# Optimization experiments

Measured on AMD Instinct MI355X. Metric: run time of the kernel, lower is better.

## Reference

```python
import jax, jax.numpy as jnp
import numpy as np

N_NODES = 100000
N_GRAPHS = 512
NEG_SLOPE = 0.2


def gat_layer(x, src, dst, W, a_src, a_dst, b):
    # PyG GATConv (heads=1, concat=True, add_self_loops handled by caller via src/dst)
    h = x @ W                                   # [N, F]
    e = jax.nn.leaky_relu((h @ a_src)[src] + (h @ a_dst)[dst], NEG_SLOPE)  # [E]
    m = jax.ops.segment_max(e, dst, num_segments=N_NODES)
    ex = jnp.exp(e - m[dst])
    s = jax.ops.segment_sum(ex, dst, num_segments=N_NODES)
    alpha = ex / (s[dst] + 1e-16)               # per-destination softmax
    out = jax.ops.segment_sum(alpha[:, None] * h[src], dst, num_segments=N_NODES)
    return out + b


def setup_inputs() -> dict:
    key = jax.random.key(0)
    ks = jax.random.split(key, 12)
    x = jax.random.normal(ks[0], (N_NODES, 5), dtype=jnp.float32)
    edge_index = jax.random.randint(ks[1], (2, 3200000), 0, N_NODES, dtype=jnp.int64)
    batch = jnp.sort(jax.random.randint(ks[2], (N_NODES,), 0, N_GRAPHS, dtype=jnp.int64))
    def glorot(k, shape):
        lim = float(np.sqrt(6.0 / (shape[0] + shape[-1])))
        return jax.random.uniform(k, shape, jnp.float32, -lim, lim)
    return {
        "x": x, "edge_index": edge_index, "batch": batch,
        "W1": glorot(ks[3], (5, 16)), "as1": glorot(ks[4], (16,)), "ad1": glorot(ks[5], (16,)), "b1": jnp.zeros((16,), jnp.float32),
        "W2": glorot(ks[6], (16, 16)), "as2": glorot(ks[7], (16,)), "ad2": glorot(ks[8], (16,)), "b2": jnp.zeros((16,), jnp.float32),
        "Wf": glorot(ks[9], (16, 2)), "bf": jnp.zeros((2,), jnp.float32),
    }


def reference(x, edge_index, batch, W1, as1, ad1, b1, W2, as2, ad2, b2, Wf, bf):
    # add self-loops (PyG GATConv default)
    loop = jnp.arange(N_NODES, dtype=edge_index.dtype)
    src = jnp.concatenate([edge_index[0], loop])
    dst = jnp.concatenate([edge_index[1], loop])
    h = jax.nn.relu(gat_layer(x, src, dst, W1, as1, ad1, b1))
    h = jax.nn.relu(gat_layer(h, src, dst, W2, as2, ad2, b2))
    # global mean pool over graphs
    sums = jax.ops.segment_sum(h, batch, num_segments=N_GRAPHS)
    cnt = jax.ops.segment_sum(jnp.ones((N_NODES,), h.dtype), batch, num_segments=N_GRAPHS)
    pooled = sums / jnp.maximum(cnt, 1.0)[:, None]   # [G, 16]
    return pooled @ Wf + bf                          # [G, 2]
```

## Files before the change

### kernel.cpp

```cpp
#include <hip/hip_runtime.h>
#include <math.h>

#define N_NODES 100000
#define N_GRAPHS 512
#define F 16
#define NEG_SLOPE 0.2f
#define DMAX 80
#define NSLOT 64
#define NBUCK 391
#define BCAP 8704
#define EPB 16

__device__ __forceinline__ float lrelu(float v) {
    return v > 0.0f ? v : NEG_SLOPE * v;
}

__device__ __forceinline__ unsigned fkey(float f) {
    unsigned b = __float_as_uint(f);
    return (b & 0x80000000u) ? ~b : (b | 0x80000000u);
}
__device__ __forceinline__ float funkey(unsigned k) {
    unsigned b = (k & 0x80000000u) ? (k ^ 0x80000000u) : ~k;
    return __uint_as_float(b);
}

__global__ void k_prep1(const float* __restrict__ x,
                        const float* __restrict__ W1,
                        const float* __restrict__ as1,
                        const float* __restrict__ ad1,
                        float* __restrict__ h1,
                        float* __restrict__ ssrc,
                        float* __restrict__ sdst,
                        unsigned* __restrict__ cs1,
                        unsigned* __restrict__ cd1) {
    int n = blockIdx.x * blockDim.x + threadIdx.x;
    float ss = -INFINITY, sd = -INFINITY;
    if (n < N_NODES) {
        float xi[5];
#pragma unroll
        for (int i = 0; i < 5; ++i) xi[i] = x[n * 5 + i];
        ss = 0.f; sd = 0.f;
#pragma unroll
        for (int f = 0; f < F; ++f) {
            float acc = 0.f;
#pragma unroll
            for (int i = 0; i < 5; ++i) acc += xi[i] * W1[i * F + f];
            h1[n * F + f] = acc;
            ss += acc * as1[f];
            sd += acc * ad1[f];
        }
        ssrc[n] = ss;
        sdst[n] = sd;
    }
    unsigned ks = fkey(ss), kd = fkey(sd);
#pragma unroll
    for (int off = 32; off; off >>= 1) {
        ks = max(ks, (unsigned)__shfl_xor((int)ks, off, 64));
        kd = max(kd, (unsigned)__shfl_xor((int)kd, off, 64));
    }
    __shared__ unsigned ls[4], ld[4];
    int wid = threadIdx.x >> 6, lane = threadIdx.x & 63;
    if (lane == 0) { ls[wid] = ks; ld[wid] = kd; }
    __syncthreads();
    if (threadIdx.x == 0) {
        unsigned ms = ls[0], md = ld[0];
#pragma unroll
        for (int w = 1; w < 4; ++w) { ms = max(ms, ls[w]); md = max(md, ld[w]); }
        atomicMax(&cs1[blockIdx.x & (NSLOT - 1)], ms);
        atomicMax(&cd1[blockIdx.x & (NSLOT - 1)], md);
    }
}

__global__ void k_part(const int* __restrict__ esrc,
                       const int* __restrict__ edst, int E0,
                       int* __restrict__ bcur,
                       unsigned* __restrict__ bucket) {
    __shared__ int hist[NBUCK];
    __shared__ int gbase[NBUCK];
    __shared__ int off[NBUCK];
    int tbase = blockIdx.x * (blockDim.x * EPB);

    for (int i = threadIdx.x; i < NBUCK; i += blockDim.x) hist[i] = 0;
    __syncthreads();

    int rb[EPB];
    unsigned rv[EPB];
#pragma unroll
    for (int i = 0; i < EPB; ++i) {
        int e = tbase + i * blockDim.x + threadIdx.x;
        rb[i] = -1;
        if (e < E0) {
            int d = edst[e];
            int s = esrc[e];
            int b = d >> 8;
            rb[i] = b;
            rv[i] = (unsigned)s | ((unsigned)(d & 255) << 17);
            atomicAdd(&hist[b], 1);
        }
    }
    __syncthreads();

    for (int b = threadIdx.x; b < NBUCK; b += blockDim.x) {
        int h = hist[b];
        gbase[b] = h ? atomicAdd(&bcur[b], h) : 0;
        off[b] = 0;
    }
    __syncthreads();

#pragma unroll
    for (int i = 0; i < EPB; ++i) {
        int b = rb[i];
        if (b >= 0) {
            int p = gbase[b] + atomicAdd(&off[b], 1);
            if (p < BCAP) bucket[(size_t)b * BCAP + p] = rv[i];
        }
    }
}

__global__ void k_fill2(const int* __restrict__ bcur,
                        const unsigned* __restrict__ bucket,
                        int* __restrict__ col,
                        int* __restrict__ deg) {
    int b = blockIdx.x;
    __shared__ int cur[256];
    if (threadIdx.x < 256) cur[threadIdx.x] = 0;
    __syncthreads();
    int cnt = min(bcur[b], BCAP);
    const unsigned* bk = bucket + (size_t)b * BCAP;
    for (int i = threadIdx.x; i < cnt; i += blockDim.x) {
        unsigned v = __builtin_nontemporal_load(&bk[i]);
        int s = (int)(v & 0x1FFFFu);
        int dl = (int)(v >> 17);
        int r = atomicAdd(&cur[dl], 1);
        if (r < DMAX) col[((size_t)((b << 8) | dl)) * DMAX + r] = s;
    }
    __syncthreads();
    if (threadIdx.x < 256) {
        int dst = (b << 8) | threadIdx.x;
        if (dst < N_NODES) deg[dst] = min(cur[threadIdx.x], DMAX);
    }
}

__device__ __forceinline__ float gat_aggregate(int n, int lane,
                                               const int* __restrict__ deg,
                                               const int* __restrict__ col,
                                               const float* __restrict__ ssrc,
                                               const float* __restrict__ sdst,
                                               const float* __restrict__ h,
                                               const float* __restrict__ b,
                                               float c) {
    int dg = deg[n];
    size_t st = (size_t)n * DMAX;
    float sd = sdst[n];
    float acc = 0.f, ssum = 0.f;
    for (int base = 0; base < dg; base += 16) {
        int j = base + lane;
        float pe = 0.f;
        int src = 0;
        if (j < dg) {
            src = __builtin_nontemporal_load(&col[st + j]);
            pe = __expf(lrelu(ssrc[src] + sd) - c);
        }
        ssum += pe;
        int cnt = min(16, dg - base);
        for (int k = 0; k < cnt; ++k) {
            int sk = __shfl(src, k, 16);
            float pk = __shfl(pe, k, 16);
            acc += pk * h[sk * F + lane];
        }
    }
#pragma unroll
    for (int off = 8; off; off >>= 1) ssum += __shfl_xor(ssum, off, 16);
    float pes = __expf(lrelu(ssrc[n] + sd) - c);
    ssum += pes;
    acc += pes * h[n * F + lane];
    float of = acc / (ssum + 1e-16f) + b[lane];
    return of > 0.f ? of : 0.f;
}

__device__ __forceinline__ float slot_max_c(const unsigned* __restrict__ cs,
                                            const unsigned* __restrict__ cd) {
    unsigned ms = 0, md = 0;
#pragma unroll 8
    for (int i = 0; i < NSLOT; ++i) {
        ms = max(ms, cs[i]);
        md = max(md, cd[i]);
    }
    return lrelu(funkey(ms) + funkey(md));
}

__global__ void k_gather1(const int* __restrict__ deg,
                          const int* __restrict__ col,
                          const float* __restrict__ ssrc1,
                          const float* __restrict__ sdst1,
                          const float* __restrict__ h1,
                          const float* __restrict__ b1,
                          const float* __restrict__ W2,
                          const float* __restrict__ as2,
                          const float* __restrict__ ad2,
                          float* __restrict__ h2,
                          float* __restrict__ ssrc2,
                          float* __restrict__ sdst2,
                          const unsigned* __restrict__ cs1,
                          const unsigned* __restrict__ cd1,
                          unsigned* __restrict__ cs2,
                          unsigned* __restrict__ cd2) {
    int n = blockIdx.x * (blockDim.x >> 4) + (threadIdx.x >> 4);
    int lane = threadIdx.x & 15;
    float c1 = slot_max_c(cs1, cd1);
    float ho = gat_aggregate(n, lane, deg, col, ssrc1, sdst1, h1, b1, c1);

    float h2f = 0.f;
#pragma unroll
    for (int i = 0; i < F; ++i) {
        float hoi = __shfl(ho, i, 16);
        h2f += hoi * W2[i * F + lane];
    }
    h2[n * F + lane] = h2f;

    float ps = h2f * as2[lane];
    float pd = h2f * ad2[lane];
#pragma unroll
    for (int off = 8; off; off >>= 1) {
        ps += __shfl_xor(ps, off, 16);
        pd += __shfl_xor(pd, off, 16);
    }
    if (lane == 0) { ssrc2[n] = ps; sdst2[n] = pd; }

    unsigned ks = fkey(ps), kd = fkey(pd);
#pragma unroll
    for (int off = 32; off; off >>= 1) {
        ks = max(ks, (unsigned)__shfl_xor((int)ks, off, 64));
        kd = max(kd, (unsigned)__shfl_xor((int)kd, off, 64));
    }
    __shared__ unsigned ls[4], ld[4];
    int wid = threadIdx.x >> 6, wl = threadIdx.x & 63;
    if (wl == 0) { ls[wid] = ks; ld[wid] = kd; }
    __syncthreads();
    if (threadIdx.x == 0) {
        unsigned ms = ls[0], md = ld[0];
#pragma unroll
        for (int w = 1; w < 4; ++w) { ms = max(ms, ls[w]); md = max(md, ld[w]); }
        atomicMax(&cs2[blockIdx.x & (NSLOT - 1)], ms);
        atomicMax(&cd2[blockIdx.x & (NSLOT - 1)], md);
    }
}

__global__ void k_gather2(const int* __restrict__ deg,
                          const int* __restrict__ col,
                          const float* __restrict__ ssrc2,
                          const float* __restrict__ sdst2,
                          const float* __restrict__ h2,
                          const float* __restrict__ b2,
                          const int* __restrict__ batch,
                          float* __restrict__ gsum,
                          float* __restrict__ gcnt,
                          const unsigned* __restrict__ cs2,
                          const unsigned* __restrict__ cd2) {
    __shared__ float pool[4 * F];
    __shared__ float pcnt[4];
    if (threadIdx.x < 4 * F) pool[threadIdx.x] = 0.f;
    if (threadIdx.x < 4) pcnt[threadIdx.x] = 0.f;
    __syncthreads();

    int n = blockIdx.x * (blockDim.x >> 4) + (threadIdx.x >> 4);
    int lane = threadIdx.x & 15;
    float c2 = slot_max_c(cs2, cd2);
    float ho = gat_aggregate(n, lane, deg, col, ssrc2, sdst2, h2, b2, c2);

    int g = batch[n];
    int g0 = batch[blockIdx.x * (blockDim.x >> 4)];
    int idx = g - g0;
    if (idx < 4) {
        atomicAdd(&pool[idx * F + lane], ho);
        if (lane == 0) atomicAdd(&pcnt[idx], 1.f);
    } else {
        atomicAdd(&gsum[g * F + lane], ho);
        if (lane == 0) atomicAdd(&gcnt[g], 1.f);
    }
    __syncthreads();
    if (threadIdx.x < 4 * F) {
        float v = pool[threadIdx.x];
        if (v != 0.f)
            atomicAdd(&gsum[(g0 + (threadIdx.x >> 4)) * F + (threadIdx.x & 15)], v);
    }
    if (threadIdx.x < 4) {
        float cv = pcnt[threadIdx.x];
        if (cv != 0.f) atomicAdd(&gcnt[g0 + threadIdx.x], cv);
    }
}

__global__ void k_final(const float* __restrict__ gsum,
                        const float* __restrict__ gcnt,
                        const float* __restrict__ Wf,
                        const float* __restrict__ bf,
                        float* __restrict__ out) {
    int g = blockIdx.x * blockDim.x + threadIdx.x;
    if (g >= N_GRAPHS) return;
    float inv = 1.f / fmaxf(gcnt[g], 1.f);
    float o0 = bf[0], o1 = bf[1];
#pragma unroll
    for (int i = 0; i < F; ++i) {
        float p = gsum[g * F + i] * inv;
        o0 += p * Wf[i * 2 + 0];
        o1 += p * Wf[i * 2 + 1];
    }
    out[g * 2 + 0] = o0;
    out[g * 2 + 1] = o1;
}

extern "C" void kernel_launch(void* const* d_in, const int* in_sizes, int n_in,
                              void* d_out, int out_size, void* d_ws, size_t ws_size,
                              hipStream_t stream) {
    const float* x   = (const float*)d_in[0];
    const int*   ei  = (const int*)d_in[1];
    const int*   bat = (const int*)d_in[2];
    const float* W1  = (const float*)d_in[3];
    const float* as1 = (const float*)d_in[4];
    const float* ad1 = (const float*)d_in[5];
    const float* b1  = (const float*)d_in[6];
    const float* W2  = (const float*)d_in[7];
    const float* as2 = (const float*)d_in[8];
    const float* ad2 = (const float*)d_in[9];
    const float* b2  = (const float*)d_in[10];
    const float* Wf  = (const float*)d_in[11];
    const float* bf  = (const float*)d_in[12];
    float* out = (float*)d_out;

    const int E0 = in_sizes[1] / 2;
    const int* esrc = ei;
    const int* edst = ei + E0;

    float* fws   = (float*)d_ws;
    float* h1    = fws;
    float* h2    = h1 + (size_t)N_NODES * F;
    float* ssrc1 = h2 + (size_t)N_NODES * F;
    float* sdst1 = ssrc1 + N_NODES;
    float* ssrc2 = sdst1 + N_NODES;
    float* sdst2 = ssrc2 + N_NODES;
    int*   col   = (int*)(sdst2 + N_NODES);
    int*   deg   = col + (size_t)N_NODES * DMAX;
    unsigned* bucket = (unsigned*)(deg + N_NODES);
    int*      zbase = (int*)(bucket + (size_t)NBUCK * BCAP);
    int*      bcur  = zbase;
    unsigned* cs1   = (unsigned*)(bcur + NBUCK);
    unsigned* cd1   = cs1 + NSLOT;
    unsigned* cs2   = cd1 + NSLOT;
    unsigned* cd2   = cs2 + NSLOT;
    float*    gsum  = (float*)(cd2 + NSLOT);
    float*    gcnt  = gsum + (size_t)N_GRAPHS * F;
    size_t zbytes = (size_t)(NBUCK + 4 * NSLOT + N_GRAPHS * F + N_GRAPHS) * 4;

    hipMemsetAsync(zbase, 0, zbytes, stream);

    const int BT = 256;
    dim3 bN((N_NODES + BT - 1) / BT);
    dim3 bT((E0 + BT * EPB - 1) / (BT * EPB));
    dim3 bB(NBUCK);
    dim3 bG16((N_NODES * 16) / BT);
    dim3 bG((N_GRAPHS + BT - 1) / BT);

    k_prep1<<<bN, BT, 0, stream>>>(x, W1, as1, ad1, h1, ssrc1, sdst1, cs1, cd1);
    k_part<<<bT, BT, 0, stream>>>(esrc, edst, E0, bcur, bucket);
    k_fill2<<<bB, 1024, 0, stream>>>(bcur, bucket, col, deg);
    k_gather1<<<bG16, BT, 0, stream>>>(deg, col, ssrc1, sdst1, h1, b1,
                                       W2, as2, ad2, h2, ssrc2, sdst2,
                                       cs1, cd1, cs2, cd2);
    k_gather2<<<bG16, BT, 0, stream>>>(deg, col, ssrc2, sdst2, h2, b2,
                                       bat, gsum, gcnt, cs2, cd2);
    k_final<<<bG, BT, 0, stream>>>(gsum, gcnt, Wf, bf, out);
}
```

Before: 330.2 us.

## Use wave-per-node float4 gather aggregation and fuse prep into partition kernel

```diff
diff --git a/kernel.cpp b/kernel.cpp
--- a/kernel.cpp
+++ b/kernel.cpp
@@ -24,95 +24,96 @@
     return __uint_as_float(b);
 }
 
-__global__ void k_prep1(const float* __restrict__ x,
-                        const float* __restrict__ W1,
-                        const float* __restrict__ as1,
-                        const float* __restrict__ ad1,
-                        float* __restrict__ h1,
-                        float* __restrict__ ssrc,
-                        float* __restrict__ sdst,
-                        unsigned* __restrict__ cs1,
-                        unsigned* __restrict__ cd1) {
-    int n = blockIdx.x * blockDim.x + threadIdx.x;
-    float ss = -INFINITY, sd = -INFINITY;
-    if (n < N_NODES) {
-        float xi[5];
-#pragma unroll
-        for (int i = 0; i < 5; ++i) xi[i] = x[n * 5 + i];
-        ss = 0.f; sd = 0.f;
-#pragma unroll
-        for (int f = 0; f < F; ++f) {
-            float acc = 0.f;
-#pragma unroll
-            for (int i = 0; i < 5; ++i) acc += xi[i] * W1[i * F + f];
-            h1[n * F + f] = acc;
-            ss += acc * as1[f];
-            sd += acc * ad1[f];
-        }
-        ssrc[n] = ss;
-        sdst[n] = sd;
-    }
-    unsigned ks = fkey(ss), kd = fkey(sd);
-#pragma unroll
-    for (int off = 32; off; off >>= 1) {
-        ks = max(ks, (unsigned)__shfl_xor((int)ks, off, 64));
-        kd = max(kd, (unsigned)__shfl_xor((int)kd, off, 64));
-    }
-    __shared__ unsigned ls[4], ld[4];
-    int wid = threadIdx.x >> 6, lane = threadIdx.x & 63;
-    if (lane == 0) { ls[wid] = ks; ld[wid] = kd; }
-    __syncthreads();
-    if (threadIdx.x == 0) {
-        unsigned ms = ls[0], md = ld[0];
-#pragma unroll
-        for (int w = 1; w < 4; ++w) { ms = max(ms, ls[w]); md = max(md, ld[w]); }
-        atomicMax(&cs1[blockIdx.x & (NSLOT - 1)], ms);
-        atomicMax(&cd1[blockIdx.x & (NSLOT - 1)], md);
-    }
-}
-
-__global__ void k_part(const int* __restrict__ esrc,
-                       const int* __restrict__ edst, int E0,
-                       int* __restrict__ bcur,
-                       unsigned* __restrict__ bucket) {
+__global__ void k_part_prep(const int* __restrict__ esrc,
+                            const int* __restrict__ edst, int E0, int nT,
+                            int* __restrict__ bcur,
+                            unsigned* __restrict__ bucket,
+                            const float* __restrict__ x,
+                            const float* __restrict__ W1,
+                            const float* __restrict__ as1,
+                            const float* __restrict__ ad1,
+                            float* __restrict__ h1,
+                            float* __restrict__ ssrc,
+                            float* __restrict__ sdst,
+                            unsigned* __restrict__ cs1,
+                            unsigned* __restrict__ cd1) {
     __shared__ int hist[NBUCK];
     __shared__ int gbase[NBUCK];
     __shared__ int off[NBUCK];
-    int tbase = blockIdx.x * (blockDim.x * EPB);
-
-    for (int i = threadIdx.x; i < NBUCK; i += blockDim.x) hist[i] = 0;
-    __syncthreads();
-
-    int rb[EPB];
-    unsigned rv[EPB];
-#pragma unroll
-    for (int i = 0; i < EPB; ++i) {
-        int e = tbase + i * blockDim.x + threadIdx.x;
-        rb[i] = -1;
-        if (e < E0) {
-            int d = edst[e];
-            int s = esrc[e];
-            int b = d >> 8;
-            rb[i] = b;
-            rv[i] = (unsigned)s | ((unsigned)(d & 255) << 17);
-            atomicAdd(&hist[b], 1);
-        }
-    }
-    __syncthreads();
-
-    for (int b = threadIdx.x; b < NBUCK; b += blockDim.x) {
-        int h = hist[b];
-        gbase[b] = h ? atomicAdd(&bcur[b], h) : 0;
-        off[b] = 0;
-    }
-    __syncthreads();
-
-#pragma unroll
-    for (int i = 0; i < EPB; ++i) {
-        int b = rb[i];
-        if (b >= 0) {
-            int p = gbase[b] + atomicAdd(&off[b], 1);
-            if (p < BCAP) bucket[(size_t)b * BCAP + p] = rv[i];
+    __shared__ unsigned ls[4], ld[4];
+
+    if ((int)blockIdx.x < nT) {
+        int tbase = blockIdx.x * (blockDim.x * EPB);
+        for (int i = threadIdx.x; i < NBUCK; i += blockDim.x) hist[i] = 0;
+        __syncthreads();
+
+        int rb[EPB];
+        unsigned rv[EPB];
+#pragma unroll
+        for (int i = 0; i < EPB; ++i) {
+            int e = tbase + i * blockDim.x + threadIdx.x;
+            rb[i] = -1;
+            if (e < E0) {
+                int d = edst[e];
+                int s = esrc[e];
+                int b = d >> 8;
+                rb[i] = b;
+                rv[i] = (unsigned)s | ((unsigned)(d & 255) << 17);
+                atomicAdd(&hist[b], 1);
+            }
+        }
+        __syncthreads();
+
+        for (int b = threadIdx.x; b < NBUCK; b += blockDim.x) {
+            int h = hist[b];
+            gbase[b] = h ? atomicAdd(&bcur[b], h) : 0;
+            off[b] = 0;
+        }
+        __syncthreads();
+
+#pragma unroll
+        for (int i = 0; i < EPB; ++i) {
+            int b = rb[i];
+            if (b >= 0) {
+                int p = gbase[b] + atomicAdd(&off[b], 1);
+                if (p < BCAP) bucket[(size_t)b * BCAP + p] = rv[i];
+            }
+        }
+    } else {
+        int n = (blockIdx.x - nT) * blockDim.x + threadIdx.x;
+        float ss = -INFINITY, sd = -INFINITY;
+        if (n < N_NODES) {
+            float xi[5];
+#pragma unroll
+            for (int i = 0; i < 5; ++i) xi[i] = x[n * 5 + i];
+            ss = 0.f; sd = 0.f;
+#pragma unroll
+            for (int f = 0; f < F; ++f) {
+                float acc = 0.f;
+#pragma unroll
+                for (int i = 0; i < 5; ++i) acc += xi[i] * W1[i * F + f];
+                h1[n * F + f] = acc;
+                ss += acc * as1[f];
+                sd += acc * ad1[f];
+            }
+            ssrc[n] = ss;
+            sdst[n] = sd;
+        }
+        unsigned ks = fkey(ss), kd = fkey(sd);
+#pragma unroll
+        for (int o = 32; o; o >>= 1) {
+            ks = max(ks, (unsigned)__shfl_xor((int)ks, o, 64));
+            kd = max(kd, (unsigned)__shfl_xor((int)kd, o, 64));
+        }
+        int wid = threadIdx.x >> 6, lane = threadIdx.x & 63;
+        if (lane == 0) { ls[wid] = ks; ld[wid] = kd; }
+        __syncthreads();
+        if (threadIdx.x == 0) {
+            unsigned ms = ls[0], md = ld[0];
+#pragma unroll
+            for (int w = 1; w < 4; ++w) { ms = max(ms, ls[w]); md = max(md, ld[w]); }
+            atomicMax(&cs1[blockIdx.x & (NSLOT - 1)], ms);
+            atomicMax(&cd1[blockIdx.x & (NSLOT - 1)], md);
         }
     }
 }
@@ -141,41 +142,55 @@
     }
 }
 
-__device__ __forceinline__ float gat_aggregate(int n, int lane,
+__device__ __forceinline__ float4 gat_agg_wave(int n, int eslot, int quad,
                                                const int* __restrict__ deg,
                                                const int* __restrict__ col,
                                                const float* __restrict__ ssrc,
                                                const float* __restrict__ sdst,
-                                               const float* __restrict__ h,
+                                               const float4* __restrict__ h4,
                                                const float* __restrict__ b,
                                                float c) {
     int dg = deg[n];
     size_t st = (size_t)n * DMAX;
     float sd = sdst[n];
-    float acc = 0.f, ssum = 0.f;
+    float4 acc = make_float4(0.f, 0.f, 0.f, 0.f);
+    float psum = 0.f;
     for (int base = 0; base < dg; base += 16) {
-        int j = base + lane;
-        float pe = 0.f;
-        int src = 0;
+        int j = base + eslot;
         if (j < dg) {
-            src = __builtin_nontemporal_load(&col[st + j]);
-            pe = __expf(lrelu(ssrc[src] + sd) - c);
-        }
-        ssum += pe;
-        int cnt = min(16, dg - base);
-        for (int k = 0; k < cnt; ++k) {
-            int sk = __shfl(src, k, 16);
-            float pk = __shfl(pe, k, 16);
-            acc += pk * h[sk * F + lane];
-        }
-    }
-#pragma unroll
-    for (int off = 8; off; off >>= 1) ssum += __shfl_xor(ssum, off, 16);
+            int src = __builtin_nontemporal_load(&col[st + j]);
+            float pe = __expf(lrelu(ssrc[src] + sd) - c);
+            float4 hv = h4[(size_t)src * 4 + quad];
+            acc.x += pe * hv.x;
+            acc.y += pe * hv.y;
+            acc.z += pe * hv.z;
+            acc.w += pe * hv.w;
+            psum += pe;
+        }
+    }
+#pragma unroll
+    for (int o = 4; o < 64; o <<= 1) {
+        acc.x += __shfl_xor(acc.x, o, 64);
+        acc.y += __shfl_xor(acc.y, o, 64);
+        acc.z += __shfl_xor(acc.z, o, 64);
+        acc.w += __shfl_xor(acc.w, o, 64);
+        psum  += __shfl_xor(psum, o, 64);
+    }
     float pes = __expf(lrelu(ssrc[n] + sd) - c);
-    ssum += pes;
-    acc += pes * h[n * F + lane];
-    float of = acc / (ssum + 1e-16f) + b[lane];
-    return of > 0.f ? of : 0.f;
+    float4 hv = h4[(size_t)n * 4 + quad];
+    acc.x += pes * hv.x;
+    acc.y += pes * hv.y;
+    acc.z += pes * hv.z;
+    acc.w += pes * hv.w;
+    psum += pes;
+    float inv = 1.f / (psum + 1e-16f);
+    const float4 bq = ((const float4*)b)[quad];
+    float4 of;
+    of.x = fmaxf(acc.x * inv + bq.x, 0.f);
+    of.y = fmaxf(acc.y * inv + bq.y, 0.f);
+    of.z = fmaxf(acc.z * inv + bq.z, 0.f);
+    of.w = fmaxf(acc.w * inv + bq.w, 0.f);
+    return of;
 }
 
 __device__ __forceinline__ float slot_max_c(const unsigned* __restrict__ cs,
@@ -205,42 +220,42 @@
                           const unsigned* __restrict__ cd1,
                           unsigned* __restrict__ cs2,
                           unsigned* __restrict__ cd2) {
-    int n = blockIdx.x * (blockDim.x >> 4) + (threadIdx.x >> 4);
-    int lane = threadIdx.x & 15;
+    __shared__ float lho[4][16];
+    __shared__ unsigned ls[4], ld[4];
+    int w = threadIdx.x >> 6;
+    int lane = threadIdx.x & 63;
+    int eslot = lane >> 2, quad = lane & 3;
+    int n = blockIdx.x * 4 + w;
+
     float c1 = slot_max_c(cs1, cd1);
-    float ho = gat_aggregate(n, lane, deg, col, ssrc1, sdst1, h1, b1, c1);
-
+    float4 of = gat_agg_wave(n, eslot, quad, deg, col, ssrc1, sdst1,
+                             (const float4*)h1, b1, c1);
+    if (eslot == 0) *(float4*)&lho[w][quad * 4] = of;
+    __syncthreads();
+
+    int f = lane & 15;
     float h2f = 0.f;
 #pragma unroll
-    for (int i = 0; i < F; ++i) {
-        float hoi = __shfl(ho, i, 16);
-        h2f += hoi * W2[i * F + lane];
-    }
-    h2[n * F + lane] = h2f;
-
-    float ps = h2f * as2[lane];
-    float pd = h2f * ad2[lane];
-#pragma unroll
-    for (int off = 8; off; off >>= 1) {
-        ps += __shfl_xor(ps, off, 16);
-        pd += __shfl_xor(pd, off, 16);
-    }
+    for (int i = 0; i < 16; ++i) h2f += lho[w][i] * W2[i * F + f];
+    if (lane < 16) h2[n * F + f] = h2f;
+
+    float ps = h2f * as2[f];
+    float pd = h2f * ad2[f];
+#pragma unroll
+    for (int o = 1; o < 64; o <<= 1) {
+        ps += __shfl_xor(ps, o, 64);
+        pd += __shfl_xor(pd, o, 64);
+    }
+    ps *= 0.25f;
+    pd *= 0.25f;
     if (lane == 0) { ssrc2[n] = ps; sdst2[n] = pd; }
 
     unsigned ks = fkey(ps), kd = fkey(pd);
-#pragma unroll
-    for (int off = 32; off; off >>= 1) {
-        ks = max(ks, (unsigned)__shfl_xor((int)ks, off, 64));
-        kd = max(kd, (unsigned)__shfl_xor((int)kd, off, 64));
-    }
-    __shared__ unsigned ls[4], ld[4];
-    int wid = threadIdx.x >> 6, wl = threadIdx.x & 63;
-    if (wl == 0) { ls[wid] = ks; ld[wid] = kd; }
+    if (lane == 0) { ls[w] = ks; ld[w] = kd; }
     __syncthreads();
     if (threadIdx.x == 0) {
-        unsigned ms = ls[0], md = ld[0];
-#pragma unroll
-        for (int w = 1; w < 4; ++w) { ms = max(ms, ls[w]); md = max(md, ld[w]); }
+        unsigned ms = max(max(ls[0], ls[1]), max(ls[2], ls[3]));
+        unsigned md = max(max(ld[0], ld[1]), max(ld[2], ld[3]));
         atomicMax(&cs2[blockIdx.x & (NSLOT - 1)], ms);
         atomicMax(&cd2[blockIdx.x & (NSLOT - 1)], md);
     }
@@ -263,20 +278,32 @@
     if (threadIdx.x < 4) pcnt[threadIdx.x] = 0.f;
     __syncthreads();
 
-    int n = blockIdx.x * (blockDim.x >> 4) + (threadIdx.x >> 4);
-    int lane = threadIdx.x & 15;
+    int w = threadIdx.x >> 6;
+    int lane = threadIdx.x & 63;
+    int eslot = lane >> 2, quad = lane & 3;
+    int n = blockIdx.x * 4 + w;
+
     float c2 = slot_max_c(cs2, cd2);
-    float ho = gat_aggregate(n, lane, deg, col, ssrc2, sdst2, h2, b2, c2);
+    float4 of = gat_agg_wave(n, eslot, quad, deg, col, ssrc2, sdst2,
+                             (const float4*)h2, b2, c2);
 
     int g = batch[n];
-    int g0 = batch[blockIdx.x * (blockDim.x >> 4)];
+    int g0 = batch[blockIdx.x * 4];
     int idx = g - g0;
-    if (idx < 4) {
-        atomicAdd(&pool[idx * F + lane], ho);
-        if (lane == 0) atomicAdd(&pcnt[idx], 1.f);
-    } else {
-        atomicAdd(&gsum[g * F + lane], ho);
-        if (lane == 0) atomicAdd(&gcnt[g], 1.f);
+    if (eslot == 0) {
+        if (idx < 4) {
+            atomicAdd(&pool[idx * F + quad * 4 + 0], of.x);
+            atomicAdd(&pool[idx * F + quad * 4 + 1], of.y);
+            atomicAdd(&pool[idx * F + quad * 4 + 2], of.z);
+            atomicAdd(&pool[idx * F + quad * 4 + 3], of.w);
+            if (quad == 0) atomicAdd(&pcnt[idx], 1.f);
+        } else {
+            atomicAdd(&gsum[g * F + quad * 4 + 0], of.x);
+            atomicAdd(&gsum[g * F + quad * 4 + 1], of.y);
+            atomicAdd(&gsum[g * F + quad * 4 + 2], of.z);
+            atomicAdd(&gsum[g * F + quad * 4 + 3], of.w);
+            if (quad == 0) atomicAdd(&gcnt[g], 1.f);
+        }
     }
     __syncthreads();
     if (threadIdx.x < 4 * F) {
@@ -354,19 +381,20 @@
     hipMemsetAsync(zbase, 0, zbytes, stream);
 
     const int BT = 256;
-    dim3 bN((N_NODES + BT - 1) / BT);
-    dim3 bT((E0 + BT * EPB - 1) / (BT * EPB));
+    const int nT = (E0 + BT * EPB - 1) / (BT * EPB);
+    const int nN = (N_NODES + BT - 1) / BT;
+    dim3 bPP(nT + nN);
     dim3 bB(NBUCK);
-    dim3 bG16((N_NODES * 16) / BT);
+    dim3 bW(N_NODES / 4);
     dim3 bG((N_GRAPHS + BT - 1) / BT);
 
-    k_prep1<<<bN, BT, 0, stream>>>(x, W1, as1, ad1, h1, ssrc1, sdst1, cs1, cd1);
-    k_part<<<bT, BT, 0, stream>>>(esrc, edst, E0, bcur, bucket);
+    k_part_prep<<<bPP, BT, 0, stream>>>(esrc, edst, E0, nT, bcur, bucket,
+                                        x, W1, as1, ad1, h1, ssrc1, sdst1, cs1, cd1);
     k_fill2<<<bB, 1024, 0, stream>>>(bcur, bucket, col, deg);
-    k_gather1<<<bG16, BT, 0, stream>>>(deg, col, ssrc1, sdst1, h1, b1,
-                                       W2, as2, ad2, h2, ssrc2, sdst2,
-                                       cs1, cd1, cs2, cd2);
-    k_gather2<<<bG16, BT, 0, stream>>>(deg, col, ssrc2, sdst2, h2, b2,
-                                       bat, gsum, gcnt, cs2, cd2);
+    k_gather1<<<bW, BT, 0, stream>>>(deg, col, ssrc1, sdst1, h1, b1,
+                                     W2, as2, ad2, h2, ssrc2, sdst2,
+                                     cs1, cd1, cs2, cd2);
+    k_gather2<<<bW, BT, 0, stream>>>(deg, col, ssrc2, sdst2, h2, b2,
+                                     bat, gsum, gcnt, cs2, cd2);
     k_final<<<bG, BT, 0, stream>>>(gsum, gcnt, Wf, bf, out);
 }
```

Result: slower. 381.0 us (+15.4%).
